# Optimization experiments

Hardware: AMD Instinct MI355X
Metric: run time of the kernel (lower is better)

## Reference

```python
import jax, jax.numpy as jnp
import numpy as np
from itertools import permutations

NODE, BATCH, DIM, STEP = 32, 64, 32, 8
E = NODE * (NODE - 1)          # 992 directed edges (all ordered pairs)
K = 3                          # edge types
MSG_HID = 64; MSG_OUT = 64; N_HID = 64; PRED_LEN = 8


def setup_inputs() -> dict:
    key = jax.random.key(0)
    ks = jax.random.split(key, 12)
    es = jnp.asarray(np.array(list(permutations(range(NODE), 2))).T, dtype=jnp.int32)  # [2, E]
    x = jax.random.normal(ks[0], (BATCH, NODE, DIM, STEP), jnp.float32)
    z = jax.nn.softmax(jax.random.normal(ks[1], (BATCH, E, K), jnp.float32), axis=-1)
    p = lambda k, shape: jax.random.normal(k, shape, jnp.float32) * 0.1
    return dict(
        x=x, z=z, es=es,
        nodes_mask=jnp.zeros((NODE,), jnp.float32),
        edges_mask=jnp.zeros((E,), jnp.float32),
        mask=jnp.zeros((1,), jnp.float32),
        msg_W1=p(ks[2], (K, 2 * DIM, MSG_HID)), msg_b1=jnp.zeros((K, MSG_HID), jnp.float32),
        msg_W2=p(ks[3], (K, MSG_HID, MSG_OUT)), msg_b2=jnp.zeros((K, MSG_OUT), jnp.float32),
        out_W1=p(ks[4], (DIM + MSG_OUT, N_HID)), out_b1=jnp.zeros((N_HID,), jnp.float32),
        out_W2=p(ks[5], (N_HID, N_HID)), out_b2=jnp.zeros((N_HID,), jnp.float32),
        out_W3=p(ks[6], (N_HID, DIM)), out_b3=jnp.zeros((DIM,), jnp.float32),
        ge_Wi=p(ks[7], (3, N_HID, N_HID)), ge_bi=jnp.zeros((3, N_HID), jnp.float32),
        ge_Wh=p(ks[8], (3, N_HID, N_HID)), ge_bh=jnp.zeros((3, N_HID), jnp.float32),
        gn_Wi=p(ks[9], (3, N_HID + DIM, N_HID + DIM)), gn_bi=jnp.zeros((3, N_HID + DIM), jnp.float32),
        gn_Wh=p(ks[10], (3, N_HID + DIM, N_HID + DIM)), gn_bh=jnp.zeros((3, N_HID + DIM), jnp.float32),
    )


def _gru(inp, hid, Wi, bi, Wh, bh):
    # GRUX: state defaults to hidden
    r = jax.nn.sigmoid(inp @ Wi[0] + bi[0] + hid @ Wh[0] + bh[0])
    i = jax.nn.sigmoid(inp @ Wi[1] + bi[1] + hid @ Wh[1] + bh[1])
    n = jnp.tanh(inp @ Wi[2] + bi[2] + r * (hid @ Wh[2] + bh[2]))
    return (1.0 - i) * n + i * hid


def _run(x, z, es, msg_W1, msg_b1, msg_W2, msg_b2,
         out_W1, out_b1, out_W2, out_b2, out_W3, out_b3,
         ge_Wi, ge_bi, ge_Wh, ge_bh, gn_Wi, gn_bi, gn_Wh, gn_bh):
    xp = jnp.transpose(x, (1, 0, 3, 2))   # [node, batch, step, dim]
    zp = jnp.transpose(z, (1, 0, 2))      # [E, batch, K]
    col, row = es[0], es[1]               # 'o2i': col,row = es; aggregate at col
    counts = jnp.clip(jax.ops.segment_sum(jnp.ones((E,), x.dtype), col, num_segments=NODE), 1.0)
    h_node = h_edge = None
    x_m = None
    xs = []
    for t in range(STEP + PRED_LEN):
        x_in = xp[:, :, t, :] if t < STEP else x_m   # [node, batch, dim]
        # edge gather: msg = cat([x[row], x[col]])
        msg = jnp.concatenate([x_in[row], x_in[col]], axis=-1)  # [E, b, 2*dim]
        # per-edge-type 2-layer MLP mixture, weighted by z, normalized by K
        h1 = jax.nn.relu(jnp.einsum('ebi,kih->kebh', msg, msg_W1) + msg_b1[:, None, None, :])
        h2 = jax.nn.relu(jnp.einsum('kebh,kho->kebo', h1, msg_W2) + msg_b2[:, None, None, :])
        msgs = jnp.einsum('kebo,ebk->ebo', h2, zp) / K          # [E, b, msg_out]
        if h_edge is not None:
            msgs = _gru(msgs, h_edge, ge_Wi, ge_bi, ge_Wh, ge_bh)
        # scatter-mean to nodes
        agg = jax.ops.segment_sum(msgs, col, num_segments=NODE) / counts[:, None, None]
        cat = jnp.concatenate([x_in, agg], axis=-1)             # [node, b, dim+msg_out]
        if h_node is not None:
            cat = _gru(cat, h_node, gn_Wi, gn_bi, gn_Wh, gn_bh)
        h = jax.nn.relu(cat @ out_W1 + out_b1)
        h = jax.nn.relu(h @ out_W2 + out_b2)
        delta = h @ out_W3 + out_b3
        x_m = x_in + delta
        h_node, h_edge = cat, msgs
        xs.append(x_m)
    x_hat = jnp.transpose(jnp.stack(xs, axis=2), (1, 0, 3, 2))  # [batch, node, dim, T]
    return x_hat


def reference(x, z, es, nodes_mask, edges_mask, mask,
              msg_W1, msg_b1, msg_W2, msg_b2,
              out_W1, out_b1, out_W2, out_b2, out_W3, out_b3,
              ge_Wi, ge_bi, ge_Wh, ge_bh, gn_Wi, gn_bi, gn_Wh, gn_bh):
    x_hat = _run(x, z, es, msg_W1, msg_b1, msg_W2, msg_b2,
                 out_W1, out_b1, out_W2, out_b2, out_W3, out_b3,
                 ge_Wi, ge_bi, ge_Wh, ge_bh, gn_Wi, gn_bi, gn_Wh, gn_bh)
    return (x_hat[:, :, :, -PRED_LEN:], x_hat, x_hat)
```

## Files before the change

### kernel.cpp

```cpp
#include <hip/hip_runtime.h>
#include <hip/hip_bf16.h>

#define NNODE 32
#define NB    64
#define NDIM  32
#define NSTEP 8
#define NE    992
#define NTT   16

typedef __bf16 bf16;
typedef __attribute__((ext_vector_type(8))) __bf16 bf16x8;
typedef __attribute__((ext_vector_type(4))) __bf16 bf16x4;
typedef __attribute__((ext_vector_type(4))) float  f32x4;

__device__ __forceinline__ f32x4 mfma_bf16(bf16x8 a, bf16x8 b, f32x4 c) {
  return __builtin_amdgcn_mfma_f32_16x16x32_bf16(a, b, c, 0, 0, 0);
}
__device__ __forceinline__ float sigm(float x) { return 1.0f / (1.0f + __expf(-x)); }
__device__ __forceinline__ float tanh_f(float x) {
  x = fminf(fmaxf(x, -15.0f), 15.0f);
  float e = __expf(2.0f * x);
  return (e - 1.0f) / (e + 1.0f);
}

__global__ void prep_weights(
    const float* __restrict__ msgW1, const float* __restrict__ msgW2,
    const float* __restrict__ geWi,  const float* __restrict__ geWh,
    const float* __restrict__ gnWi,  const float* __restrict__ gnWh,
    const float* __restrict__ oW1,   const float* __restrict__ oW2,
    const float* __restrict__ oW3,
    bf16* __restrict__ B1, bf16* __restrict__ B2,
    bf16* __restrict__ GI, bf16* __restrict__ GH,
    bf16* __restrict__ GN,
    bf16* __restrict__ OW1s, bf16* __restrict__ OW2s, bf16* __restrict__ OW3s) {
  int u = blockIdx.x * 256 + threadIdx.x;
  if (u < 12288) {
    int k = u >> 12, i = (u >> 6) & 63, h = u & 63;
// ... 21 lines not shown
    OW1s[((nt * 3 + kf) * 64 + lane) * 8 + j] = (bf16)oW1[v];
  } else if (u < 50176) {
    int v = u - 46080; int i = v >> 6, h = v & 63;
    int kf = i >> 5, quad = (i >> 3) & 3, j = i & 7;
    int nt = h >> 4, lane = quad * 16 + (h & 15);
    OW2s[((nt * 2 + kf) * 64 + lane) * 8 + j] = (bf16)oW2[v];
  } else if (u < 52224) {
    int v = u - 50176; int i = v >> 5, h = v & 31;
    int kf = i >> 5, quad = (i >> 3) & 3, j = i & 7;
    int nt = h >> 4, lane = quad * 16 + (h & 15);
    OW3s[((nt * 2 + kf) * 64 + lane) * 8 + j] = (bf16)oW3[v];
  }
}

__global__ void copy_x(const float* __restrict__ x, float* __restrict__ xf,
                       bf16* __restrict__ xb) {
  int u = blockIdx.x * 256 + threadIdx.x;
  int n = u >> 11, b = (u >> 5) & 63, d = u & 31;
  float v = x[((b * 32 + n) * 32 + d) * 8 + 0];
  xf[u] = v;
  xb[u] = (bf16)v;
}

__global__ __launch_bounds__(512, 4) void edge_step(
    const bf16* __restrict__ xb, const int* __restrict__ es,
    const float* __restrict__ z,
    const bf16* __restrict__ B1, const bf16* __restrict__ B2,
    const float* __restrict__ mb1, const float* __restrict__ mb2,
    const bf16* __restrict__ GI, const bf16* __restrict__ GH,
    const float* __restrict__ gbi, const float* __restrict__ gbh,
    bf16* __restrict__ hed, int t) {
  __shared__ __align__(16) char scrbuf[51200];
  __shared__ float zL[2][64][3];
  __shared__ float biasL[768];
  bf16 (*A)[64][72]   = (bf16(*)[64][72])scrbuf;
  bf16 (*A2)[64][200] = (bf16(*)[64][200])scrbuf;

  int e0 = blockIdx.x * 2, tid = threadIdx.x;
  int c0_ = es[e0],     r0 = es[NE + e0];
  int c1_ = es[e0 + 1], r1 = es[NE + e0 + 1];
  for (int u = tid; u < 768; u += 512)
    biasL[u] = (u < 192) ? mb1[u] : (u < 384) ? mb2[u - 192]
             : (u < 576) ? gbi[u - 384] : gbh[u - 576];
  for (int u = tid; u < 384; u += 512) {
    int pe = u / 192, rem = u % 192, b = rem / 3, k = rem % 3;
    zL[pe][b][k] = z[(b * NE + e0 + pe) * 3 + k];
  }
  for (int u = tid; u < 1024; u += 512) {
    int pe = u >> 9, c = u & 511;
    int b = c >> 3, i8 = c & 7;
    int nrow = pe ? r1 : r0, ncol = pe ? c1_ : c0_;
    const bf16* src = (i8 < 4) ? (xb + nrow * 2048 + b * 32 + i8 * 8)
                               : (xb + ncol * 2048 + b * 32 + (i8 - 4) * 8);
    *(bf16x8*)&A[pe][b][i8 * 8] = *(const bf16x8*)src;
  }
  __syncthreads();
  int wv = tid >> 6, ln = tid & 63, quad = ln >> 4, l16 = ln & 15;
  int rg = wv & 3, cg = wv >> 2;
  int m = rg * 16 + l16;
  bf16x8 af[2][2];
#pragma unroll
  for (int pe = 0; pe < 2; pe++)
#pragma unroll
    for (int kf = 0; kf < 2; kf++)
      af[pe][kf] = *(const bf16x8*)&A[pe][m][kf * 32 + quad * 8];
  __syncthreads();
  f32x4 acc1[2][6];
#pragma unroll
  for (int pe = 0; pe < 2; pe++)
#pragma unroll
    for (int q = 0; q < 6; q++) { f32x4 zz = {0.f,0.f,0.f,0.f}; acc1[pe][q] = zz; }
#pragma unroll
  for (int j = 0; j < 6; j++) {
    int nt = cg * 6 + j;
    bf16x8 w0 = *(const bf16x8*)&B1[(nt * 2 + 0) * 512 + ln * 8];
    bf16x8 w1 = *(const bf16x8*)&B1[(nt * 2 + 1) * 512 + ln * 8];
#pragma unroll
    for (int pe = 0; pe < 2; pe++) {
      acc1[pe][j] = mfma_bf16(af[pe][0], w0, acc1[pe][j]);
      acc1[pe][j] = mfma_bf16(af[pe][1], w1, acc1[pe][j]);
    }
  }
#pragma unroll
  for (int j = 0; j < 6; j++) {
    int nt = cg * 6 + j;
    int n = nt * 16 + l16;
    float bias = biasL[n];
#pragma unroll
    for (int pe = 0; pe < 2; pe++)
#pragma unroll
      for (int r = 0; r < 4; r++) {
        float v = acc1[pe][j][r] + bias;
        A2[pe][rg * 16 + quad * 4 + r][n] = (bf16)(v > 0.f ? v : 0.f);
      }
  }
  __syncthreads();
  f32x4 acc2[2][3][2];
#pragma unroll
  for (int pe = 0; pe < 2; pe++)
#pragma unroll
    for (int kt = 0; kt < 3; kt++)
#pragma unroll
      for (int oi = 0; oi < 2; oi++) { f32x4 zz = {0.f,0.f,0.f,0.f}; acc2[pe][kt][oi] = zz; }
#pragma unroll
  for (int kt = 0; kt < 3; kt++) {
    bf16x8 a2f[2][2];
#pragma unroll
    for (int pe = 0; pe < 2; pe++)
#pragma unroll
      for (int kf = 0; kf < 2; kf++)
        a2f[pe][kf] = *(const bf16x8*)&A2[pe][m][kt * 64 + kf * 32 + quad * 8];
#pragma unroll
    for (int oi = 0; oi < 2; oi++) {
      int ot = cg * 2 + oi;
      bf16x8 w0 = *(const bf16x8*)&B2[kt * 4096 + (ot * 2 + 0) * 512 + ln * 8];
      bf16x8 w1 = *(const bf16x8*)&B2[kt * 4096 + (ot * 2 + 1) * 512 + ln * 8];
#pragma unroll
      for (int pe = 0; pe < 2; pe++) {
        acc2[pe][kt][oi] = mfma_bf16(a2f[pe][0], w0, acc2[pe][kt][oi]);
        acc2[pe][kt][oi] = mfma_bf16(a2f[pe][1], w1, acc2[pe][kt][oi]);
      }
    }
  }
  __syncthreads();
#pragma unroll
  for (int pe = 0; pe < 2; pe++)
#pragma unroll
    for (int r = 0; r < 4; r++) {
      int b = rg * 16 + quad * 4 + r;
      float z0 = zL[pe][b][0], z1 = zL[pe][b][1], z2 = zL[pe][b][2];
#pragma unroll
      for (int oi = 0; oi < 2; oi++) {
        int o = (cg * 2 + oi) * 16 + l16;
        float h0 = acc2[pe][0][oi][r] + biasL[192 + o];       h0 = h0 > 0.f ? h0 : 0.f;
        float h1 = acc2[pe][1][oi][r] + biasL[192 + 64 + o];  h1 = h1 > 0.f ? h1 : 0.f;
        float h2 = acc2[pe][2][oi][r] + biasL[192 + 128 + o]; h2 = h2 > 0.f ? h2 : 0.f;
        A[pe][b][o] = (bf16)((h0 * z0 + h1 * z1 + h2 * z2) * (1.0f / 3.0f));
      }
    }
  if (t > 0) {
    __syncthreads();
    bf16x8 ai[2][2], ah[2][2];
#pragma unroll
    for (int pe = 0; pe < 2; pe++) {
      const bf16* hrow = hed + (e0 + pe) * 4096 + m * 64;
#pragma unroll
      for (int kf = 0; kf < 2; kf++) {
        ai[pe][kf] = *(const bf16x8*)&A[pe][m][kf * 32 + quad * 8];
        ah[pe][kf] = *(const bf16x8*)(hrow + kf * 32 + quad * 8);
      }
    }
#pragma unroll
    for (int oi = 0; oi < 2; oi++) {
      int ot = cg * 2 + oi;
      f32x4 gr[2], gi2[2], gni2[2], gnh2[2];
#pragma unroll
      for (int pe = 0; pe < 2; pe++) {
        f32x4 zz = {0.f,0.f,0.f,0.f};
        gr[pe] = zz; gi2[pe] = zz; gni2[pe] = zz; gnh2[pe] = zz;
      }
#pragma unroll
      for (int g = 0; g < 2; g++) {
        int nt = g * 4 + ot;
        bf16x8 wi0 = *(const bf16x8*)&GI[(nt * 2 + 0) * 512 + ln * 8];
        bf16x8 wi1 = *(const bf16x8*)&GI[(nt * 2 + 1) * 512 + ln * 8];
        bf16x8 wh0 = *(const bf16x8*)&GH[(nt * 2 + 0) * 512 + ln * 8];
        bf16x8 wh1 = *(const bf16x8*)&GH[(nt * 2 + 1) * 512 + ln * 8];
#pragma unroll
        for (int pe = 0; pe < 2; pe++) {
          f32x4 a = g ? gi2[pe] : gr[pe];
          a = mfma_bf16(ai[pe][0], wi0, a);
          a = mfma_bf16(ai[pe][1], wi1, a);
          a = mfma_bf16(ah[pe][0], wh0, a);
          a = mfma_bf16(ah[pe][1], wh1, a);
          if (g) gi2[pe] = a; else gr[pe] = a;
        }
      }
      {
        int nt = 8 + ot;
        bf16x8 wi0 = *(const bf16x8*)&GI[(nt * 2 + 0) * 512 + ln * 8];
        bf16x8 wi1 = *(const bf16x8*)&GI[(nt * 2 + 1) * 512 + ln * 8];
        bf16x8 wh0 = *(const bf16x8*)&GH[(nt * 2 + 0) * 512 + ln * 8];
        bf16x8 wh1 = *(const bf16x8*)&GH[(nt * 2 + 1) * 512 + ln * 8];
#pragma unroll
        for (int pe = 0; pe < 2; pe++) {
          gni2[pe] = mfma_bf16(ai[pe][0], wi0, gni2[pe]);
          gni2[pe] = mfma_bf16(ai[pe][1], wi1, gni2[pe]);
          gnh2[pe] = mfma_bf16(ah[pe][0], wh0, gnh2[pe]);
          gnh2[pe] = mfma_bf16(ah[pe][1], wh1, gnh2[pe]);
        }
      }
#pragma unroll
      for (int pe = 0; pe < 2; pe++)
#pragma unroll
        for (int r = 0; r < 4; r++) {
          int b = rg * 16 + quad * 4 + r;
          int o = ot * 16 + l16;
          float xr = gr[pe][r]   + biasL[384 + o]       + biasL[576 + o];
          float xi = gi2[pe][r]  + biasL[384 + 64 + o]  + biasL[576 + 64 + o];
          float xn = gni2[pe][r] + biasL[384 + 128 + o];
          float hn = gnh2[pe][r] + biasL[576 + 128 + o];
          float rgt = sigm(xr);
          float ig  = sigm(xi);
          float ng  = tanh_f(xn + rgt * hn);
          float hv  = (float)hed[(e0 + pe) * 4096 + b * 64 + o];
          A[pe][b][o] = (bf16)((1.0f - ig) * ng + ig * hv);
        }
    }
  }
  __syncthreads();
  for (int u = tid; u < 1024; u += 512) {
    int pe = u >> 9, c = u & 511;
    int b = c >> 3, j = c & 7;
    *(bf16x8*)(hed + (e0 + pe) * 4096 + b * 64 + j * 8) = *(const bf16x8*)&A[pe][b][j * 8];
  }
}

__global__ __launch_bounds__(256) void node_kernel(
    const float* __restrict__ x, const bf16* __restrict__ hed,
    float* __restrict__ xf, bf16* __restrict__ xb, float* __restrict__ hnode,
    const bf16* __restrict__ GN,
    const float* __restrict__ gnbi, const float* __restrict__ gnbh,
    const bf16* __restrict__ OW1, const float* __restrict__ ob1,
    const bf16* __restrict__ OW2, const float* __restrict__ ob2,
    const bf16* __restrict__ OW3, const float* __restrict__ ob3,
    float* __restrict__ out, int t) {
  __shared__ float aggf[16][64];
  __shared__ float xinf[16][32];
  __shared__ float hvf[16][96];
  __shared__ __align__(16) bf16 c0b[16][112];
  __shared__ __align__(16) bf16 hvb[16][112];
  __shared__ float gsum[2][16][290];
  __shared__ __align__(16) bf16 cnb[16][112];
  __shared__ __align__(16) bf16 s1b[16][112];
  __shared__ __align__(16) bf16 s2b[16][112];
  int nq = blockIdx.x, n = nq >> 2, q = nq & 3;
  int tid = threadIdx.x;
  {
    int r = tid >> 4, o4 = tid & 15;
    const bf16x4* bp = (const bf16x4*)hed + (size_t)n * 31 * 1024 + (q * 16 + r) * 16 + o4;
    float sx = 0.f, sy = 0.f, sz = 0.f, sw = 0.f;
#pragma unroll
    for (int e2 = 0; e2 < 31; e2++) {
      bf16x4 v = bp[e2 * 1024];
      sx += (float)v[0]; sy += (float)v[1]; sz += (float)v[2]; sw += (float)v[3];
    }
    const float inv = 1.0f / 31.0f;
    sx *= inv; sy *= inv; sz *= inv; sw *= inv;
    int o = o4 * 4;
    aggf[r][o] = sx; aggf[r][o + 1] = sy; aggf[r][o + 2] = sz; aggf[r][o + 3] = sw;
    c0b[r][32 + o] = (bf16)sx; c0b[r][33 + o] = (bf16)sy;
    c0b[r][34 + o] = (bf16)sz; c0b[r][35 + o] = (bf16)sw;
  }
  if (tid < 128) {
    int r = tid >> 3, d0 = (tid & 7) * 4;
    int b = q * 16 + r;
#pragma unroll
    for (int k = 0; k < 4; k++) {
      float v = xf[n * 2048 + b * 32 + d0 + k];
      xinf[r][d0 + k] = v;
      c0b[r][d0 + k] = (bf16)v;
    }
  }
  if (t > 0) {
    int r = tid >> 4, cb = (tid & 15) * 6;
    int row = n * 64 + q * 16 + r;
#pragma unroll
    for (int k = 0; k < 6; k++) {
      float v = hnode[row * 96 + cb + k];
      hvf[r][cb + k] = v;
      hvb[r][cb + k] = (bf16)v;
    }
  }
  __syncthreads();
  int wv = tid >> 6, ln = tid & 63, quad = ln >> 4, l16 = ln & 15;
  if (t > 0) {
    int mat = wv >> 1, sel = wv & 1;
    const bf16(*Ab)[112] = mat ? hvb : c0b;
    bf16x8 af[3];
#pragma unroll
    for (int kf = 0; kf < 3; kf++)
      af[kf] = *(const bf16x8*)&Ab[l16][kf * 32 + quad * 8];
    const bf16* W = GN + mat * 27648;
    f32x4 accn[9];
#pragma unroll
    for (int q2 = 0; q2 < 9; q2++) { f32x4 zz = {0.f,0.f,0.f,0.f}; accn[q2] = zz; }
#pragma unroll
    for (int nt2 = 0; nt2 < 9; nt2++) {
      int nt = sel * 9 + nt2;
#pragma unroll
      for (int kf = 0; kf < 3; kf++) {
        bf16x8 bfrag = *(const bf16x8*)&W[((nt * 3 + kf) * 64 + ln) * 8];
        accn[nt2] = mfma_bf16(af[kf], bfrag, accn[nt2]);
      }
    }
#pragma unroll
    for (int nt2 = 0; nt2 < 9; nt2++) {
      int col = (sel * 9 + nt2) * 16 + l16;
#pragma unroll
      for (int rr = 0; rr < 4; rr++)
        gsum[mat][quad * 4 + rr][col] = accn[nt2][rr];
    }
  }
  __syncthreads();
  {
    int r = tid >> 4, cb = (tid & 15) * 6;
    int row = n * 64 + q * 16 + r;
#pragma unroll
    for (int k = 0; k < 6; k++) {
      int c = cb + k;
      float v;
      if (t > 0) {
        float xr = gsum[0][r][c] + gnbi[c] + gsum[1][r][c] + gnbh[c];
        float xi = gsum[0][r][96 + c] + gnbi[96 + c] + gsum[1][r][96 + c] + gnbh[96 + c];
        float xn = gsum[0][r][192 + c] + gnbi[192 + c];
        float hn = gsum[1][r][192 + c] + gnbh[192 + c];
        float rg = sigm(xr);
        float ig = sigm(xi);
        float ng = tanh_f(xn + rg * hn);
        v = (1.0f - ig) * ng + ig * hvf[r][c];
      } else {
        v = (c < 32) ? xinf[r][c] : aggf[r][c - 32];
      }
      cnb[r][c] = (bf16)v;
      hnode[row * 96 + c] = v;
    }
  }
  __syncthreads();
  {
    bf16x8 af[3];
#pragma unroll
    for (int kf = 0; kf < 3; kf++)
      af[kf] = *(const bf16x8*)&cnb[l16][kf * 32 + quad * 8];
    f32x4 accn = {0.f, 0.f, 0.f, 0.f};
#pragma unroll
    for (int kf = 0; kf < 3; kf++) {
      bf16x8 bfrag = *(const bf16x8*)&OW1[((wv * 3 + kf) * 64 + ln) * 8];
      accn = mfma_bf16(af[kf], bfrag, accn);
    }
    int col = wv * 16 + l16;
    float bias = ob1[col];
#pragma unroll
    for (int rr = 0; rr < 4; rr++) {
      float vv = accn[rr] + bias;
      s1b[quad * 4 + rr][col] = (bf16)(vv > 0.f ? vv : 0.f);
    }
  }
  __syncthreads();
  {
    bf16x8 af[2];
#pragma unroll
    for (int kf = 0; kf < 2; kf++)
      af[kf] = *(const bf16x8*)&s1b[l16][kf * 32 + quad * 8];
    f32x4 accn = {0.f, 0.f, 0.f, 0.f};
#pragma unroll
    for (int kf = 0; kf < 2; kf++) {
      bf16x8 bfrag = *(const bf16x8*)&OW2[((wv * 2 + kf) * 64 + ln) * 8];
      accn = mfma_bf16(af[kf], bfrag, accn);
    }
    int col = wv * 16 + l16;
    float bias = ob2[col];
#pragma unroll
    for (int rr = 0; rr < 4; rr++) {
      float vv = accn[rr] + bias;
      s2b[quad * 4 + rr][col] = (bf16)(vv > 0.f ? vv : 0.f);
    }
  }
  __syncthreads();
  if (wv < 2) {
    bf16x8 af[2];
#pragma unroll
    for (int kf = 0; kf < 2; kf++)
      af[kf] = *(const bf16x8*)&s2b[l16][kf * 32 + quad * 8];
    f32x4 accn = {0.f, 0.f, 0.f, 0.f};
#pragma unroll
    for (int kf = 0; kf < 2; kf++) {
      bf16x8 bfrag = *(const bf16x8*)&OW3[((wv * 2 + kf) * 64 + ln) * 8];
      accn = mfma_bf16(af[kf], bfrag, accn);
    }
    int d = wv * 16 + l16;
    float bias = ob3[d];
#pragma unroll
    for (int rr = 0; rr < 4; rr++) {
      int r = quad * 4 + rr;
      int b = q * 16 + r;
      float xm = xinf[r][d] + accn[rr] + bias;
      int base = (b * 32 + n) * 32 + d;
      out[524288 + base * 16 + t] = xm;
      out[1572864 + base * 16 + t] = xm;
      if (t >= NSTEP) out[base * 8 + (t - NSTEP)] = xm;
      float vnext = (t + 1 < NSTEP) ? x[base * 8 + (t + 1)] : xm;
      xf[n * 2048 + b * 32 + d] = vnext;
      xb[n * 2048 + b * 32 + d] = (bf16)vnext;
    }
  }
}

extern "C" void kernel_launch(void* const* d_in, const int* in_sizes, int n_in,
                              void* d_out, int out_size, void* d_ws, size_t ws_size,
                              hipStream_t stream) {
  const float* x     = (const float*)d_in[0];
  const float* z     = (const float*)d_in[1];
  const int*   es    = (const int*)d_in[2];
  const float* msgW1 = (const float*)d_in[6];
  const float* msgb1 = (const float*)d_in[7];
  const float* msgW2 = (const float*)d_in[8];
  const float* msgb2 = (const float*)d_in[9];
  const float* oW1   = (const float*)d_in[10];
  const float* ob1   = (const float*)d_in[11];
// ... 12 lines not shown
  float* out = (float*)d_out;

  char* p = (char*)d_ws;
  bf16*  hed   = (bf16*)p;   p += (size_t)NE * 4096 * 2;
  float* xf    = (float*)p;  p += 65536 * 4;
  bf16*  xb    = (bf16*)p;   p += 65536 * 2;
  float* hnode = (float*)p;  p += 196608 * 4;
  bf16*  B1sw  = (bf16*)p;   p += 12288 * 2;
  bf16*  B2sw  = (bf16*)p;   p += 12288 * 2;
  bf16*  GIsw  = (bf16*)p;   p += 12288 * 2;
  bf16*  GHsw  = (bf16*)p;   p += 12288 * 2;
  bf16*  GNsw  = (bf16*)p;   p += 55296 * 2;
  bf16*  OW1s  = (bf16*)p;   p += 6144 * 2;
  bf16*  OW2s  = (bf16*)p;   p += 4096 * 2;
  bf16*  OW3s  = (bf16*)p;   p += 2048 * 2;

  prep_weights<<<204, 256, 0, stream>>>(msgW1, msgW2, geWi, geWh, gnWi, gnWh,
                                        oW1, oW2, oW3,
                                        B1sw, B2sw, GIsw, GHsw, GNsw,
                                        OW1s, OW2s, OW3s);
  copy_x<<<256, 256, 0, stream>>>(x, xf, xb);

  for (int t = 0; t < NTT; t++) {
    edge_step<<<NE / 2, 512, 0, stream>>>(xb, es, z, B1sw, B2sw, msgb1, msgb2,
                                          GIsw, GHsw, gebi, gebh, hed, t);
    node_kernel<<<128, 256, 0, stream>>>(x, hed, xf, xb, hnode, GNsw, gnbi, gnbh,
                                         OW1s, ob1, OW2s, ob2, OW3s, ob3,
                                         out, t);
  }
}
```

Measured before the change: 614.2 us.

## Fuse per-step edge and node kernels into one persistent kernel with grid barrier

Replaces the 32 alternating edge_step/node_kernel launches with a single persistent kernel of 496 blocks that loops over all 16 timesteps and synchronises through a hierarchical atomic grid barrier. Node work is folded into the same blocks, and biases plus the z values are loaded into shared memory once for the whole loop. This removes per-launch overhead and inter-kernel gaps. The cost is that all blocks must be co-resident, which risks deadlock if occupancy is insufficient, and every block pays for barrier spin-waiting.

```diff
diff --git a/kernel.cpp b/kernel.cpp
--- a/kernel.cpp
+++ b/kernel.cpp
@@ -7,6 +7,7 @@
 #define NSTEP 8
 #define NE    992
 #define NTT   16
+#define NBLK  496
 
 typedef __bf16 bf16;
 typedef __attribute__((ext_vector_type(8))) __bf16 bf16x8;
@@ -21,6 +22,26 @@
   x = fminf(fmaxf(x, -15.0f), 15.0f);
   float e = __expf(2.0f * x);
   return (e - 1.0f) / (e + 1.0f);
+}
+
+__device__ __forceinline__ void grid_barrier(unsigned* bar, unsigned phase) {
+  __syncthreads();
+  if (threadIdx.x == 0) {
+    __threadfence();
+    unsigned* leafc = bar + (blockIdx.x & 15) * 32;
+    unsigned* rootc = bar + 512;
+    unsigned* gen   = bar + 544;
+    unsigned a = __hip_atomic_fetch_add(leafc, 1u, __ATOMIC_ACQ_REL, __HIP_MEMORY_SCOPE_AGENT);
+    if (a + 1 == phase * 31u) {
+      unsigned rb = __hip_atomic_fetch_add(rootc, 1u, __ATOMIC_ACQ_REL, __HIP_MEMORY_SCOPE_AGENT);
+      if (rb + 1 == phase * 16u)
+        __hip_atomic_store(gen, phase, __ATOMIC_RELEASE, __HIP_MEMORY_SCOPE_AGENT);
+    }
+    while (__hip_atomic_load(gen, __ATOMIC_RELAXED, __HIP_MEMORY_SCOPE_AGENT) < phase)
+      __builtin_amdgcn_s_sleep(2);
+    __threadfence();
+  }
+  __syncthreads();
 }
 
 __global__ void prep_weights(
@@ -72,385 +93,421 @@
 }
 
 __global__ void copy_x(const float* __restrict__ x, float* __restrict__ xf,
-                       bf16* __restrict__ xb) {
+                       bf16* __restrict__ xb, unsigned* __restrict__ bar) {
   int u = blockIdx.x * 256 + threadIdx.x;
+  if (u < 576) bar[u] = 0u;
   int n = u >> 11, b = (u >> 5) & 63, d = u & 31;
   float v = x[((b * 32 + n) * 32 + d) * 8 + 0];
   xf[u] = v;
   xb[u] = (bf16)v;
 }
 
-__global__ __launch_bounds__(512, 4) void edge_step(
-    const bf16* __restrict__ xb, const int* __restrict__ es,
+__global__ __launch_bounds__(512, 4) void fused_rnn(
+    const float* __restrict__ x, const int* __restrict__ es,
     const float* __restrict__ z,
     const bf16* __restrict__ B1, const bf16* __restrict__ B2,
     const float* __restrict__ mb1, const float* __restrict__ mb2,
     const bf16* __restrict__ GI, const bf16* __restrict__ GH,
     const float* __restrict__ gbi, const float* __restrict__ gbh,
-    bf16* __restrict__ hed, int t) {
-  __shared__ __align__(16) char scrbuf[51200];
-  __shared__ float zL[2][64][3];
-  __shared__ float biasL[768];
-  bf16 (*A)[64][72]   = (bf16(*)[64][72])scrbuf;
-  bf16 (*A2)[64][200] = (bf16(*)[64][200])scrbuf;
-
-  int e0 = blockIdx.x * 2, tid = threadIdx.x;
-  int c0_ = es[e0],     r0 = es[NE + e0];
-  int c1_ = es[e0 + 1], r1 = es[NE + e0 + 1];
-  for (int u = tid; u < 768; u += 512)
-    biasL[u] = (u < 192) ? mb1[u] : (u < 384) ? mb2[u - 192]
-             : (u < 576) ? gbi[u - 384] : gbh[u - 576];
-  for (int u = tid; u < 384; u += 512) {
-    int pe = u / 192, rem = u % 192, b = rem / 3, k = rem % 3;
-    zL[pe][b][k] = z[(b * NE + e0 + pe) * 3 + k];
-  }
-  for (int u = tid; u < 1024; u += 512) {
-    int pe = u >> 9, c = u & 511;
-    int b = c >> 3, i8 = c & 7;
-    int nrow = pe ? r1 : r0, ncol = pe ? c1_ : c0_;
-    const bf16* src = (i8 < 4) ? (xb + nrow * 2048 + b * 32 + i8 * 8)
-                               : (xb + ncol * 2048 + b * 32 + (i8 - 4) * 8);
-    *(bf16x8*)&A[pe][b][i8 * 8] = *(const bf16x8*)src;
-  }
-  __syncthreads();
-  int wv = tid >> 6, ln = tid & 63, quad = ln >> 4, l16 = ln & 15;
-  int rg = wv & 3, cg = wv >> 2;
-  int m = rg * 16 + l16;
-  bf16x8 af[2][2];
-#pragma unroll
-  for (int pe = 0; pe < 2; pe++)
-#pragma unroll
-    for (int kf = 0; kf < 2; kf++)
-      af[pe][kf] = *(const bf16x8*)&A[pe][m][kf * 32 + quad * 8];
-  __syncthreads();
-  f32x4 acc1[2][6];
-#pragma unroll
-  for (int pe = 0; pe < 2; pe++)
-#pragma unroll
-    for (int q = 0; q < 6; q++) { f32x4 zz = {0.f,0.f,0.f,0.f}; acc1[pe][q] = zz; }
-#pragma unroll
-  for (int j = 0; j < 6; j++) {
-    int nt = cg * 6 + j;
-    bf16x8 w0 = *(const bf16x8*)&B1[(nt * 2 + 0) * 512 + ln * 8];
-    bf16x8 w1 = *(const bf16x8*)&B1[(nt * 2 + 1) * 512 + ln * 8];
-#pragma unroll
-    for (int pe = 0; pe < 2; pe++) {
-      acc1[pe][j] = mfma_bf16(af[pe][0], w0, acc1[pe][j]);
-      acc1[pe][j] = mfma_bf16(af[pe][1], w1, acc1[pe][j]);
-    }
-  }
-#pragma unroll
-  for (int j = 0; j < 6; j++) {
-    int nt = cg * 6 + j;
-    int n = nt * 16 + l16;
-    float bias = biasL[n];
-#pragma unroll
-    for (int pe = 0; pe < 2; pe++)
-#pragma unroll
-      for (int r = 0; r < 4; r++) {
-        float v = acc1[pe][j][r] + bias;
-        A2[pe][rg * 16 + quad * 4 + r][n] = (bf16)(v > 0.f ? v : 0.f);
-      }
-  }
-  __syncthreads();
-  f32x4 acc2[2][3][2];
-#pragma unroll
-  for (int pe = 0; pe < 2; pe++)
-#pragma unroll
-    for (int kt = 0; kt < 3; kt++)
-#pragma unroll
-      for (int oi = 0; oi < 2; oi++) { f32x4 zz = {0.f,0.f,0.f,0.f}; acc2[pe][kt][oi] = zz; }
-#pragma unroll
-  for (int kt = 0; kt < 3; kt++) {
-    bf16x8 a2f[2][2];
-#pragma unroll
-    for (int pe = 0; pe < 2; pe++)
-#pragma unroll
-      for (int kf = 0; kf < 2; kf++)
-        a2f[pe][kf] = *(const bf16x8*)&A2[pe][m][kt * 64 + kf * 32 + quad * 8];
-#pragma unroll
-    for (int oi = 0; oi < 2; oi++) {
-      int ot = cg * 2 + oi;
-      bf16x8 w0 = *(const bf16x8*)&B2[kt * 4096 + (ot * 2 + 0) * 512 + ln * 8];
-      bf16x8 w1 = *(const bf16x8*)&B2[kt * 4096 + (ot * 2 + 1) * 512 + ln * 8];
-#pragma unroll
-      for (int pe = 0; pe < 2; pe++) {
-        acc2[pe][kt][oi] = mfma_bf16(a2f[pe][0], w0, acc2[pe][kt][oi]);
-        acc2[pe][kt][oi] = mfma_bf16(a2f[pe][1], w1, acc2[pe][kt][oi]);
-      }
-    }
-  }
-  __syncthreads();
-#pragma unroll
-  for (int pe = 0; pe < 2; pe++)
-#pragma unroll
-    for (int r = 0; r < 4; r++) {
-      int b = rg * 16 + quad * 4 + r;
-      float z0 = zL[pe][b][0], z1 = zL[pe][b][1], z2 = zL[pe][b][2];
-#pragma unroll
-      for (int oi = 0; oi < 2; oi++) {
-        int o = (cg * 2 + oi) * 16 + l16;
-        float h0 = acc2[pe][0][oi][r] + biasL[192 + o];       h0 = h0 > 0.f ? h0 : 0.f;
-        float h1 = acc2[pe][1][oi][r] + biasL[192 + 64 + o];  h1 = h1 > 0.f ? h1 : 0.f;
-        float h2 = acc2[pe][2][oi][r] + biasL[192 + 128 + o]; h2 = h2 > 0.f ? h2 : 0.f;
-        A[pe][b][o] = (bf16)((h0 * z0 + h1 * z1 + h2 * z2) * (1.0f / 3.0f));
-      }
-    }
-  if (t > 0) {
-    __syncthreads();
-    bf16x8 ai[2][2], ah[2][2];
-#pragma unroll
-    for (int pe = 0; pe < 2; pe++) {
-      const bf16* hrow = hed + (e0 + pe) * 4096 + m * 64;
-#pragma unroll
-      for (int kf = 0; kf < 2; kf++) {
-        ai[pe][kf] = *(const bf16x8*)&A[pe][m][kf * 32 + quad * 8];
-        ah[pe][kf] = *(const bf16x8*)(hrow + kf * 32 + quad * 8);
-      }
-    }
-#pragma unroll
-    for (int oi = 0; oi < 2; oi++) {
-      int ot = cg * 2 + oi;
-      f32x4 gr[2], gi2[2], gni2[2], gnh2[2];
-#pragma unroll
-      for (int pe = 0; pe < 2; pe++) {
-        f32x4 zz = {0.f,0.f,0.f,0.f};
-        gr[pe] = zz; gi2[pe] = zz; gni2[pe] = zz; gnh2[pe] = zz;
-      }
-#pragma unroll
-      for (int g = 0; g < 2; g++) {
-        int nt = g * 4 + ot;
-        bf16x8 wi0 = *(const bf16x8*)&GI[(nt * 2 + 0) * 512 + ln * 8];
-        bf16x8 wi1 = *(const bf16x8*)&GI[(nt * 2 + 1) * 512 + ln * 8];
-        bf16x8 wh0 = *(const bf16x8*)&GH[(nt * 2 + 0) * 512 + ln * 8];
-        bf16x8 wh1 = *(const bf16x8*)&GH[(nt * 2 + 1) * 512 + ln * 8];
-#pragma unroll
-        for (int pe = 0; pe < 2; pe++) {
-          f32x4 a = g ? gi2[pe] : gr[pe];
-          a = mfma_bf16(ai[pe][0], wi0, a);
-          a = mfma_bf16(ai[pe][1], wi1, a);
-          a = mfma_bf16(ah[pe][0], wh0, a);
-          a = mfma_bf16(ah[pe][1], wh1, a);
-          if (g) gi2[pe] = a; else gr[pe] = a;
-        }
-      }
-      {
-        int nt = 8 + ot;
-        bf16x8 wi0 = *(const bf16x8*)&GI[(nt * 2 + 0) * 512 + ln * 8];
-        bf16x8 wi1 = *(const bf16x8*)&GI[(nt * 2 + 1) * 512 + ln * 8];
-        bf16x8 wh0 = *(const bf16x8*)&GH[(nt * 2 + 0) * 512 + ln * 8];
-        bf16x8 wh1 = *(const bf16x8*)&GH[(nt * 2 + 1) * 512 + ln * 8];
-#pragma unroll
-        for (int pe = 0; pe < 2; pe++) {
-          gni2[pe] = mfma_bf16(ai[pe][0], wi0, gni2[pe]);
-          gni2[pe] = mfma_bf16(ai[pe][1], wi1, gni2[pe]);
-          gnh2[pe] = mfma_bf16(ah[pe][0], wh0, gnh2[pe]);
-          gnh2[pe] = mfma_bf16(ah[pe][1], wh1, gnh2[pe]);
-        }
-      }
-#pragma unroll
-      for (int pe = 0; pe < 2; pe++)
-#pragma unroll
-        for (int r = 0; r < 4; r++) {
-          int b = rg * 16 + quad * 4 + r;
-          int o = ot * 16 + l16;
-          float xr = gr[pe][r]   + biasL[384 + o]       + biasL[576 + o];
-          float xi = gi2[pe][r]  + biasL[384 + 64 + o]  + biasL[576 + 64 + o];
-          float xn = gni2[pe][r] + biasL[384 + 128 + o];
-          float hn = gnh2[pe][r] + biasL[576 + 128 + o];
-          float rgt = sigm(xr);
-          float ig  = sigm(xi);
-          float ng  = tanh_f(xn + rgt * hn);
-          float hv  = (float)hed[(e0 + pe) * 4096 + b * 64 + o];
-          A[pe][b][o] = (bf16)((1.0f - ig) * ng + ig * hv);
-        }
-    }
-  }
-  __syncthreads();
-  for (int u = tid; u < 1024; u += 512) {
-    int pe = u >> 9, c = u & 511;
-    int b = c >> 3, j = c & 7;
-    *(bf16x8*)(hed + (e0 + pe) * 4096 + b * 64 + j * 8) = *(const bf16x8*)&A[pe][b][j * 8];
-  }
-}
-
-__global__ __launch_bounds__(256) void node_kernel(
-    const float* __restrict__ x, const bf16* __restrict__ hed,
-    float* __restrict__ xf, bf16* __restrict__ xb, float* __restrict__ hnode,
     const bf16* __restrict__ GN,
     const float* __restrict__ gnbi, const float* __restrict__ gnbh,
     const bf16* __restrict__ OW1, const float* __restrict__ ob1,
     const bf16* __restrict__ OW2, const float* __restrict__ ob2,
     const bf16* __restrict__ OW3, const float* __restrict__ ob3,
-    float* __restrict__ out, int t) {
-  __shared__ float aggf[16][64];
-  __shared__ float xinf[16][32];
-  __shared__ float hvf[16][96];
-  __shared__ __align__(16) bf16 c0b[16][112];
-  __shared__ __align__(16) bf16 hvb[16][112];
-  __shared__ float gsum[2][16][290];
-  __shared__ __align__(16) bf16 cnb[16][112];
-  __shared__ __align__(16) bf16 s1b[16][112];
-  __shared__ __align__(16) bf16 s2b[16][112];
-  int nq = blockIdx.x, n = nq >> 2, q = nq & 3;
-  int tid = threadIdx.x;
-  {
-    int r = tid >> 4, o4 = tid & 15;
-    const bf16x4* bp = (const bf16x4*)hed + (size_t)n * 31 * 1024 + (q * 16 + r) * 16 + o4;
-    float sx = 0.f, sy = 0.f, sz = 0.f, sw = 0.f;
-#pragma unroll
-    for (int e2 = 0; e2 < 31; e2++) {
-      bf16x4 v = bp[e2 * 1024];
-      sx += (float)v[0]; sy += (float)v[1]; sz += (float)v[2]; sw += (float)v[3];
-    }
-    const float inv = 1.0f / 31.0f;
-    sx *= inv; sy *= inv; sz *= inv; sw *= inv;
-    int o = o4 * 4;
-    aggf[r][o] = sx; aggf[r][o + 1] = sy; aggf[r][o + 2] = sz; aggf[r][o + 3] = sw;
-    c0b[r][32 + o] = (bf16)sx; c0b[r][33 + o] = (bf16)sy;
-    c0b[r][34 + o] = (bf16)sz; c0b[r][35 + o] = (bf16)sw;
+    bf16* __restrict__ hed, float* __restrict__ xf, bf16* __restrict__ xb,
+    float* __restrict__ hnode, float* __restrict__ out,
+    unsigned* __restrict__ bar) {
+  __shared__ __align__(16) char scrbuf[51200];
+  __shared__ float zL[2][64][3];
+  __shared__ float biasL[1504];
+  __shared__ __align__(16) bf16 hedL[2][64][72];
+
+  bf16 (*A)[64][72]   = (bf16(*)[64][72])scrbuf;
+  bf16 (*A2)[64][200] = (bf16(*)[64][200])scrbuf;
+  float (*xinf)[32]  = (float(*)[32])(scrbuf + 0);
+  float (*hvf)[96]   = (float(*)[96])(scrbuf + 2048);
+  bf16  (*c0b)[112]  = (bf16(*)[112])(scrbuf + 8192);
+  bf16  (*hvb)[112]  = (bf16(*)[112])(scrbuf + 11776);
+  float (*gri)[194]  = (float(*)[194])(scrbuf + 15360);
+  float (*gni)[98]   = (float(*)[98])(scrbuf + 27776);
+  float (*gnh)[98]   = (float(*)[98])(scrbuf + 34048);
+  bf16  (*cnb)[112]  = (bf16(*)[112])(scrbuf + 40320);
+  bf16  (*s1b)[112]  = (bf16(*)[112])(scrbuf + 43904);
+  bf16  (*s2b)[112]  = (bf16(*)[112])(scrbuf + 47488);
+  float (*aggPB)[64] = (float(*)[64])(scrbuf + 15360);
+
+  int bid = blockIdx.x, tid = threadIdx.x;
+  int e0 = bid * 2;
+  int c0_ = es[e0],     r0 = es[NE + e0];
+  int c1_ = es[e0 + 1], r1 = es[NE + e0 + 1];
+  int wv = tid >> 6, ln = tid & 63, quad = ln >> 4, l16 = ln & 15;
+  int rg = wv & 3, cg = wv >> 2;
+  int m = rg * 16 + l16;
+
+  for (int u = tid; u < 1504; u += 512) {
+    float v;
+    if      (u < 192)  v = mb1[u];
+    else if (u < 384)  v = mb2[u - 192];
+    else if (u < 576)  v = gbi[u - 384];
+    else if (u < 768)  v = gbh[u - 576];
+    else if (u < 1056) v = gnbi[u - 768];
+    else if (u < 1344) v = gnbh[u - 1056];
+    else if (u < 1408) v = ob1[u - 1344];
+    else if (u < 1472) v = ob2[u - 1408];
+    else               v = ob3[u - 1472];
+    biasL[u] = v;
   }
-  if (tid < 128) {
-    int r = tid >> 3, d0 = (tid & 7) * 4;
-    int b = q * 16 + r;
-#pragma unroll
-    for (int k = 0; k < 4; k++) {
-      float v = xf[n * 2048 + b * 32 + d0 + k];
-      xinf[r][d0 + k] = v;
-      c0b[r][d0 + k] = (bf16)v;
-    }
+  for (int u = tid; u < 384; u += 512) {
+    int pe = u / 192, rem = u % 192, b = rem / 3, k = rem % 3;
+    zL[pe][b][k] = z[(b * NE + e0 + pe) * 3 + k];
   }
-  if (t > 0) {
-    int r = tid >> 4, cb = (tid & 15) * 6;
-    int row = n * 64 + q * 16 + r;
-#pragma unroll
-    for (int k = 0; k < 6; k++) {
-      float v = hnode[row * 96 + cb + k];
-      hvf[r][cb + k] = v;
-      hvb[r][cb + k] = (bf16)v;
-    }
-  }
-  __syncthreads();
-  int wv = tid >> 6, ln = tid & 63, quad = ln >> 4, l16 = ln & 15;
-  if (t > 0) {
-    int mat = wv >> 1, sel = wv & 1;
-    const bf16(*Ab)[112] = mat ? hvb : c0b;
-    bf16x8 af[3];
-#pragma unroll
-    for (int kf = 0; kf < 3; kf++)
-      af[kf] = *(const bf16x8*)&Ab[l16][kf * 32 + quad * 8];
-    const bf16* W = GN + mat * 27648;
-    f32x4 accn[9];
-#pragma unroll
-    for (int q2 = 0; q2 < 9; q2++) { f32x4 zz = {0.f,0.f,0.f,0.f}; accn[q2] = zz; }
-#pragma unroll
-    for (int nt2 = 0; nt2 < 9; nt2++) {
-      int nt = sel * 9 + nt2;
-#pragma unroll
-      for (int kf = 0; kf < 3; kf++) {
-        bf16x8 bfrag = *(const bf16x8*)&W[((nt * 3 + kf) * 64 + ln) * 8];
-        accn[nt2] = mfma_bf16(af[kf], bfrag, accn[nt2]);
-      }
-    }
-#pragma unroll
-    for (int nt2 = 0; nt2 < 9; nt2++) {
-      int col = (sel * 9 + nt2) * 16 + l16;
-#pragma unroll
-      for (int rr = 0; rr < 4; rr++)
-        gsum[mat][quad * 4 + rr][col] = accn[nt2][rr];
-    }
-  }
-  __syncthreads();
-  {
-    int r = tid >> 4, cb = (tid & 15) * 6;
-    int row = n * 64 + q * 16 + r;
-#pragma unroll
-    for (int k = 0; k < 6; k++) {
-      int c = cb + k;
-      float v;
+
+  unsigned phase = 0;
+  for (int t = 0; t < NTT; t++) {
+    for (int u = tid; u < 1024; u += 512) {
+      int pe = u >> 9, c = u & 511;
+      int b = c >> 3, i8 = c & 7;
+      int nrow = pe ? r1 : r0, ncol = pe ? c1_ : c0_;
+      const bf16* src = (i8 < 4) ? (xb + nrow * 2048 + b * 32 + i8 * 8)
+                                 : (xb + ncol * 2048 + b * 32 + (i8 - 4) * 8);
+      *(bf16x8*)&A[pe][b][i8 * 8] = *(const bf16x8*)src;
+    }
+    __syncthreads();
+    bf16x8 af[2][2];
+#pragma unroll
+    for (int pe = 0; pe < 2; pe++)
+#pragma unroll
+      for (int kf = 0; kf < 2; kf++)
+        af[pe][kf] = *(const bf16x8*)&A[pe][m][kf * 32 + quad * 8];
+    __syncthreads();
+    f32x4 acc1[2][6];
+#pragma unroll
+    for (int pe = 0; pe < 2; pe++)
+#pragma unroll
+      for (int q2 = 0; q2 < 6; q2++) { f32x4 zz = {0.f,0.f,0.f,0.f}; acc1[pe][q2] = zz; }
+#pragma unroll
+    for (int j = 0; j < 6; j++) {
+      int nt = cg * 6 + j;
+      bf16x8 w0 = *(const bf16x8*)&B1[(nt * 2 + 0) * 512 + ln * 8];
+      bf16x8 w1 = *(const bf16x8*)&B1[(nt * 2 + 1) * 512 + ln * 8];
+#pragma unroll
+      for (int pe = 0; pe < 2; pe++) {
+        acc1[pe][j] = mfma_bf16(af[pe][0], w0, acc1[pe][j]);
+        acc1[pe][j] = mfma_bf16(af[pe][1], w1, acc1[pe][j]);
+      }
+    }
+#pragma unroll
+    for (int j = 0; j < 6; j++) {
+      int nt = cg * 6 + j;
+      int n2 = nt * 16 + l16;
+      float bias = biasL[n2];
+#pragma unroll
+      for (int pe = 0; pe < 2; pe++)
+#pragma unroll
+        for (int r = 0; r < 4; r++) {
+          float v = acc1[pe][j][r] + bias;
+          A2[pe][rg * 16 + quad * 4 + r][n2] = (bf16)(v > 0.f ? v : 0.f);
+        }
+    }
+    __syncthreads();
+    f32x4 acc2[2][3][2];
+#pragma unroll
+    for (int pe = 0; pe < 2; pe++)
+#pragma unroll
+      for (int kt = 0; kt < 3; kt++)
+#pragma unroll
+        for (int oi = 0; oi < 2; oi++) { f32x4 zz = {0.f,0.f,0.f,0.f}; acc2[pe][kt][oi] = zz; }
+#pragma unroll
+    for (int kt = 0; kt < 3; kt++) {
+      bf16x8 a2f[2][2];
+#pragma unroll
+      for (int pe = 0; pe < 2; pe++)
+#pragma unroll
+        for (int kf = 0; kf < 2; kf++)
+          a2f[pe][kf] = *(const bf16x8*)&A2[pe][m][kt * 64 + kf * 32 + quad * 8];
+#pragma unroll
+      for (int oi = 0; oi < 2; oi++) {
+        int ot = cg * 2 + oi;
+        bf16x8 w0 = *(const bf16x8*)&B2[kt * 4096 + (ot * 2 + 0) * 512 + ln * 8];
+        bf16x8 w1 = *(const bf16x8*)&B2[kt * 4096 + (ot * 2 + 1) * 512 + ln * 8];
+#pragma unroll
+        for (int pe = 0; pe < 2; pe++) {
+          acc2[pe][kt][oi] = mfma_bf16(a2f[pe][0], w0, acc2[pe][kt][oi]);
+          acc2[pe][kt][oi] = mfma_bf16(a2f[pe][1], w1, acc2[pe][kt][oi]);
+        }
+      }
+    }
+    __syncthreads();
+#pragma unroll
+    for (int pe = 0; pe < 2; pe++)
+#pragma unroll
+      for (int r = 0; r < 4; r++) {
+        int b = rg * 16 + quad * 4 + r;
+        float z0 = zL[pe][b][0], z1 = zL[pe][b][1], z2 = zL[pe][b][2];
+#pragma unroll
+        for (int oi = 0; oi < 2; oi++) {
+          int o = (cg * 2 + oi) * 16 + l16;
+          float h0 = acc2[pe][0][oi][r] + biasL[192 + o];       h0 = h0 > 0.f ? h0 : 0.f;
+          float h1 = acc2[pe][1][oi][r] + biasL[192 + 64 + o];  h1 = h1 > 0.f ? h1 : 0.f;
+          float h2 = acc2[pe][2][oi][r] + biasL[192 + 128 + o]; h2 = h2 > 0.f ? h2 : 0.f;
+          A[pe][b][o] = (bf16)((h0 * z0 + h1 * z1 + h2 * z2) * (1.0f / 3.0f));
+        }
+      }
+    if (t > 0) {
+      __syncthreads();
+      bf16x8 ai[2][2], ah[2][2];
+#pragma unroll
+      for (int pe = 0; pe < 2; pe++)
+#pragma unroll
+        for (int kf = 0; kf < 2; kf++) {
+          ai[pe][kf] = *(const bf16x8*)&A[pe][m][kf * 32 + quad * 8];
+          ah[pe][kf] = *(const bf16x8*)&hedL[pe][m][kf * 32 + quad * 8];
+        }
+#pragma unroll
+      for (int oi = 0; oi < 2; oi++) {
+        int ot = cg * 2 + oi;
+        f32x4 gr[2], gi2[2], gni2[2], gnh2[2];
+#pragma unroll
+        for (int pe = 0; pe < 2; pe++) {
+          f32x4 zz = {0.f,0.f,0.f,0.f};
+          gr[pe] = zz; gi2[pe] = zz; gni2[pe] = zz; gnh2[pe] = zz;
+        }
+#pragma unroll
+        for (int g = 0; g < 2; g++) {
+          int nt = g * 4 + ot;
+          bf16x8 wi0 = *(const bf16x8*)&GI[(nt * 2 + 0) * 512 + ln * 8];
+          bf16x8 wi1 = *(const bf16x8*)&GI[(nt * 2 + 1) * 512 + ln * 8];
+          bf16x8 wh0 = *(const bf16x8*)&GH[(nt * 2 + 0) * 512 + ln * 8];
+          bf16x8 wh1 = *(const bf16x8*)&GH[(nt * 2 + 1) * 512 + ln * 8];
+#pragma unroll
+          for (int pe = 0; pe < 2; pe++) {
+            f32x4 a = g ? gi2[pe] : gr[pe];
+            a = mfma_bf16(ai[pe][0], wi0, a);
+            a = mfma_bf16(ai[pe][1], wi1, a);
+            a = mfma_bf16(ah[pe][0], wh0, a);
+            a = mfma_bf16(ah[pe][1], wh1, a);
+            if (g) gi2[pe] = a; else gr[pe] = a;
+          }
+        }
+        {
+          int nt = 8 + ot;
+          bf16x8 wi0 = *(const bf16x8*)&GI[(nt * 2 + 0) * 512 + ln * 8];
+          bf16x8 wi1 = *(const bf16x8*)&GI[(nt * 2 + 1) * 512 + ln * 8];
+          bf16x8 wh0 = *(const bf16x8*)&GH[(nt * 2 + 0) * 512 + ln * 8];
+          bf16x8 wh1 = *(const bf16x8*)&GH[(nt * 2 + 1) * 512 + ln * 8];
+#pragma unroll
+          for (int pe = 0; pe < 2; pe++) {
+            gni2[pe] = mfma_bf16(ai[pe][0], wi0, gni2[pe]);
+            gni2[pe] = mfma_bf16(ai[pe][1], wi1, gni2[pe]);
+            gnh2[pe] = mfma_bf16(ah[pe][0], wh0, gnh2[pe]);
+            gnh2[pe] = mfma_bf16(ah[pe][1], wh1, gnh2[pe]);
+          }
+        }
+#pragma unroll
+        for (int pe = 0; pe < 2; pe++)
+#pragma unroll
+          for (int r = 0; r < 4; r++) {
+            int b = rg * 16 + quad * 4 + r;
+            int o = ot * 16 + l16;
+            float xr = gr[pe][r]   + biasL[384 + o]       + biasL[576 + o];
+            float xi = gi2[pe][r]  + biasL[384 + 64 + o]  + biasL[576 + 64 + o];
+            float xn = gni2[pe][r] + biasL[384 + 128 + o];
+            float hn = gnh2[pe][r] + biasL[576 + 128 + o];
+            float rgt = sigm(xr);
+            float ig  = sigm(xi);
+            float ng  = tanh_f(xn + rgt * hn);
+            float hv  = (float)hedL[pe][b][o];
+            A[pe][b][o] = (bf16)((1.0f - ig) * ng + ig * hv);
+          }
+      }
+    }
+    __syncthreads();
+    for (int u = tid; u < 1024; u += 512) {
+      int pe = u >> 9, c = u & 511;
+      int b = c >> 3, j = c & 7;
+      bf16x8 v = *(const bf16x8*)&A[pe][b][j * 8];
+      *(bf16x8*)(hed + (e0 + pe) * 4096 + b * 64 + j * 8) = v;
+      *(bf16x8*)&hedL[pe][b][j * 8] = v;
+    }
+
+    phase++; grid_barrier(bar, phase);
+
+    if (bid < 128) {
+      int n = bid >> 2, q = bid & 3;
+      int half = tid >> 8;
+      int r4 = (tid >> 4) & 15, o4 = tid & 15;
+      float sx = 0.f, sy = 0.f, sz2 = 0.f, sw = 0.f;
+      {
+        const bf16x4* bp = (const bf16x4*)hed + (size_t)n * 31 * 1024 +
+                           (q * 16 + r4) * 16 + o4 + (half ? (size_t)16384 : 0);
+        int ecnt = half ? 15 : 16;
+        for (int e2 = 0; e2 < ecnt; e2++) {
+          bf16x4 v = bp[(size_t)e2 * 1024];
+          sx += (float)v[0]; sy += (float)v[1]; sz2 += (float)v[2]; sw += (float)v[3];
+        }
+        if (half) {
+          f32x4 pv = {sx, sy, sz2, sw};
+          *(f32x4*)&aggPB[r4][o4 * 4] = pv;
+        }
+      }
+      if (tid < 128) {
+        int r = tid >> 3, d0 = (tid & 7) * 4;
+        int b = q * 16 + r;
+#pragma unroll
+        for (int k = 0; k < 4; k++) {
+          float v = xf[n * 2048 + b * 32 + d0 + k];
+          xinf[r][d0 + k] = v;
+          c0b[r][d0 + k] = (bf16)v;
+          if (t == 0) hnode[(n * 64 + b) * 96 + d0 + k] = v;
+        }
+      }
+      if (t > 0 && tid < 256) {
+        int r = tid >> 4, cb = (tid & 15) * 6;
+        int row = n * 64 + q * 16 + r;
+#pragma unroll
+        for (int k = 0; k < 6; k++) {
+          float v = hnode[row * 96 + cb + k];
+          hvf[r][cb + k] = v;
+          hvb[r][cb + k] = (bf16)v;
+        }
+      }
+      __syncthreads();
+      if (tid < 256) {
+        f32x4 pv = *(const f32x4*)&aggPB[r4][o4 * 4];
+        const float inv = 1.0f / 31.0f;
+        sx = (sx + pv[0]) * inv; sy = (sy + pv[1]) * inv;
+        sz2 = (sz2 + pv[2]) * inv; sw = (sw + pv[3]) * inv;
+        int o = o4 * 4;
+        c0b[r4][32 + o] = (bf16)sx; c0b[r4][33 + o] = (bf16)sy;
+        c0b[r4][34 + o] = (bf16)sz2; c0b[r4][35 + o] = (bf16)sw;
+        if (t == 0) {
+          int row = n * 64 + q * 16 + r4;
+          hnode[row * 96 + 32 + o] = sx;  hnode[row * 96 + 33 + o] = sy;
+          hnode[row * 96 + 34 + o] = sz2; hnode[row * 96 + 35 + o] = sw;
+        }
+      }
+      __syncthreads();
       if (t > 0) {
-        float xr = gsum[0][r][c] + gnbi[c] + gsum[1][r][c] + gnbh[c];
-        float xi = gsum[0][r][96 + c] + gnbi[96 + c] + gsum[1][r][96 + c] + gnbh[96 + c];
-        float xn = gsum[0][r][192 + c] + gnbi[192 + c];
-        float hn = gsum[1][r][192 + c] + gnbh[192 + c];
-        float rg = sigm(xr);
-        float ig = sigm(xi);
-        float ng = tanh_f(xn + rg * hn);
-        v = (1.0f - ig) * ng + ig * hvf[r][c];
-      } else {
-        v = (c < 32) ? xinf[r][c] : aggf[r][c - 32];
-      }
-      cnb[r][c] = (bf16)v;
-      hnode[row * 96 + c] = v;
-    }
-  }
-  __syncthreads();
-  {
-    bf16x8 af[3];
-#pragma unroll
-    for (int kf = 0; kf < 3; kf++)
-      af[kf] = *(const bf16x8*)&cnb[l16][kf * 32 + quad * 8];
-    f32x4 accn = {0.f, 0.f, 0.f, 0.f};
-#pragma unroll
-    for (int kf = 0; kf < 3; kf++) {
-      bf16x8 bfrag = *(const bf16x8*)&OW1[((wv * 3 + kf) * 64 + ln) * 8];
-      accn = mfma_bf16(af[kf], bfrag, accn);
-    }
-    int col = wv * 16 + l16;
-    float bias = ob1[col];
-#pragma unroll
-    for (int rr = 0; rr < 4; rr++) {
-      float vv = accn[rr] + bias;
-      s1b[quad * 4 + rr][col] = (bf16)(vv > 0.f ? vv : 0.f);
-    }
-  }
-  __syncthreads();
-  {
-    bf16x8 af[2];
-#pragma unroll
-    for (int kf = 0; kf < 2; kf++)
-      af[kf] = *(const bf16x8*)&s1b[l16][kf * 32 + quad * 8];
-    f32x4 accn = {0.f, 0.f, 0.f, 0.f};
-#pragma unroll
-    for (int kf = 0; kf < 2; kf++) {
-      bf16x8 bfrag = *(const bf16x8*)&OW2[((wv * 2 + kf) * 64 + ln) * 8];
-      accn = mfma_bf16(af[kf], bfrag, accn);
-    }
-    int col = wv * 16 + l16;
-    float bias = ob2[col];
-#pragma unroll
-    for (int rr = 0; rr < 4; rr++) {
-      float vv = accn[rr] + bias;
-      s2b[quad * 4 + rr][col] = (bf16)(vv > 0.f ? vv : 0.f);
-    }
-  }
-  __syncthreads();
-  if (wv < 2) {
-    bf16x8 af[2];
-#pragma unroll
-    for (int kf = 0; kf < 2; kf++)
-      af[kf] = *(const bf16x8*)&s2b[l16][kf * 32 + quad * 8];
-    f32x4 accn = {0.f, 0.f, 0.f, 0.f};
-#pragma unroll
-    for (int kf = 0; kf < 2; kf++) {
-      bf16x8 bfrag = *(const bf16x8*)&OW3[((wv * 2 + kf) * 64 + ln) * 8];
-      accn = mfma_bf16(af[kf], bfrag, accn);
-    }
-    int d = wv * 16 + l16;
-    float bias = ob3[d];
-#pragma unroll
-    for (int rr = 0; rr < 4; rr++) {
-      int r = quad * 4 + rr;
-      int b = q * 16 + r;
-      float xm = xinf[r][d] + accn[rr] + bias;
-      int base = (b * 32 + n) * 32 + d;
-      out[524288 + base * 16 + t] = xm;
-      out[1572864 + base * 16 + t] = xm;
-      if (t >= NSTEP) out[base * 8 + (t - NSTEP)] = xm;
-      float vnext = (t + 1 < NSTEP) ? x[base * 8 + (t + 1)] : xm;
-      xf[n * 2048 + b * 32 + d] = vnext;
-      xb[n * 2048 + b * 32 + d] = (bf16)vnext;
-    }
+        bf16x8 a0[3], a1[3];
+#pragma unroll
+        for (int kf = 0; kf < 3; kf++) {
+          a0[kf] = *(const bf16x8*)&c0b[l16][kf * 32 + quad * 8];
+          a1[kf] = *(const bf16x8*)&hvb[l16][kf * 32 + quad * 8];
+        }
+        for (int nt = wv; nt < 18; nt += 8) {
+          f32x4 acc0 = {0.f,0.f,0.f,0.f}, accB = {0.f,0.f,0.f,0.f};
+#pragma unroll
+          for (int kf = 0; kf < 3; kf++) {
+            bf16x8 w0 = *(const bf16x8*)&GN[((nt * 3 + kf) * 64 + ln) * 8];
+            bf16x8 w1 = *(const bf16x8*)&GN[27648 + ((nt * 3 + kf) * 64 + ln) * 8];
+            acc0 = mfma_bf16(a0[kf], w0, acc0);
+            accB = mfma_bf16(a1[kf], w1, accB);
+          }
+          int colb = nt * 16 + l16;
+          if (nt < 12) {
+#pragma unroll
+            for (int rr = 0; rr < 4; rr++)
+              gri[quad * 4 + rr][colb] = acc0[rr] + accB[rr];
+          } else {
+#pragma unroll
+            for (int rr = 0; rr < 4; rr++) {
+              gni[quad * 4 + rr][colb - 192] = acc0[rr];
+              gnh[quad * 4 + rr][colb - 192] = accB[rr];
+            }
+          }
+        }
+      }
+      __syncthreads();
+      if (t > 0 && tid < 256) {
+        int r = tid >> 4, cb = (tid & 15) * 6;
+        int row = n * 64 + q * 16 + r;
+#pragma unroll
+        for (int k = 0; k < 6; k++) {
+          int c = cb + k;
+          float xr = gri[r][c]      + biasL[768 + c]      + biasL[1056 + c];
+          float xi = gri[r][96 + c] + biasL[864 + c]      + biasL[1152 + c];
+          float xn = gni[r][c] + biasL[960 + c];
+          float hn = gnh[r][c] + biasL[1248 + c];
+          float rg2 = sigm(xr);
+          float ig = sigm(xi);
+          float ng = tanh_f(xn + rg2 * hn);
+          float v = (1.0f - ig) * ng + ig * hvf[r][c];
+          cnb[r][c] = (bf16)v;
+          hnode[row * 96 + c] = v;
+        }
+      }
+      __syncthreads();
+      const bf16 (*CN)[112] = (t > 0) ? (const bf16(*)[112])cnb : (const bf16(*)[112])c0b;
+      if (wv < 4) {
+        bf16x8 af3[3];
+#pragma unroll
+        for (int kf = 0; kf < 3; kf++)
+          af3[kf] = *(const bf16x8*)&CN[l16][kf * 32 + quad * 8];
+        f32x4 accn = {0.f,0.f,0.f,0.f};
+#pragma unroll
+        for (int kf = 0; kf < 3; kf++) {
+          bf16x8 bfrag = *(const bf16x8*)&OW1[((wv * 3 + kf) * 64 + ln) * 8];
+          accn = mfma_bf16(af3[kf], bfrag, accn);
+        }
+        int col = wv * 16 + l16;
+        float bias = biasL[1344 + col];
+#pragma unroll
+        for (int rr = 0; rr < 4; rr++) {
+          float vv = accn[rr] + bias;
+          s1b[quad * 4 + rr][col] = (bf16)(vv > 0.f ? vv : 0.f);
+        }
+      }
+      __syncthreads();
+      if (wv < 4) {
+        bf16x8 af2[2];
+#pragma unroll
+        for (int kf = 0; kf < 2; kf++)
+          af2[kf] = *(const bf16x8*)&s1b[l16][kf * 32 + quad * 8];
+        f32x4 accn = {0.f,0.f,0.f,0.f};
+#pragma unroll
+        for (int kf = 0; kf < 2; kf++) {
+          bf16x8 bfrag = *(const bf16x8*)&OW2[((wv * 2 + kf) * 64 + ln) * 8];
+          accn = mfma_bf16(af2[kf], bfrag, accn);
+        }
+        int col = wv * 16 + l16;
+        float bias = biasL[1408 + col];
+#pragma unroll
+        for (int rr = 0; rr < 4; rr++) {
+          float vv = accn[rr] + bias;
+          s2b[quad * 4 + rr][col] = (bf16)(vv > 0.f ? vv : 0.f);
+        }
+      }
+      __syncthreads();
+      if (wv < 2) {
+        bf16x8 af2[2];
+#pragma unroll
+        for (int kf = 0; kf < 2; kf++)
+          af2[kf] = *(const bf16x8*)&s2b[l16][kf * 32 + quad * 8];
+        f32x4 accn = {0.f,0.f,0.f,0.f};
+#pragma unroll
+        for (int kf = 0; kf < 2; kf++) {
+          bf16x8 bfrag = *(const bf16x8*)&OW3[((wv * 2 + kf) * 64 + ln) * 8];
+          accn = mfma_bf16(af2[kf], bfrag, accn);
+        }
+        int d = wv * 16 + l16;
+        float bias = biasL[1472 + d];
+#pragma unroll
+        for (int rr = 0; rr < 4; rr++) {
+          int r = quad * 4 + rr;
+          int b = q * 16 + r;
+          float xm = xinf[r][d] + accn[rr] + bias;
+          int base = (b * 32 + n) * 32 + d;
+          out[524288 + base * 16 + t] = xm;
+          out[1572864 + base * 16 + t] = xm;
+          if (t >= NSTEP) out[base * 8 + (t - NSTEP)] = xm;
+          float vnext = (t + 1 < NSTEP) ? x[base * 8 + (t + 1)] : xm;
+          xf[n * 2048 + b * 32 + d] = vnext;
+          xb[n * 2048 + b * 32 + d] = (bf16)vnext;
+        }
+      }
+    }
+
+    if (t < NTT - 1) { phase++; grid_barrier(bar, phase); }
   }
 }
 
@@ -493,18 +550,17 @@
   bf16*  OW1s  = (bf16*)p;   p += 6144 * 2;
   bf16*  OW2s  = (bf16*)p;   p += 4096 * 2;
   bf16*  OW3s  = (bf16*)p;   p += 2048 * 2;
+  unsigned* bar = (unsigned*)p; p += 576 * 4;
 
   prep_weights<<<204, 256, 0, stream>>>(msgW1, msgW2, geWi, geWh, gnWi, gnWh,
                                         oW1, oW2, oW3,
                                         B1sw, B2sw, GIsw, GHsw, GNsw,
                                         OW1s, OW2s, OW3s);
-  copy_x<<<256, 256, 0, stream>>>(x, xf, xb);
-
-  for (int t = 0; t < NTT; t++) {
-    edge_step<<<NE / 2, 512, 0, stream>>>(xb, es, z, B1sw, B2sw, msgb1, msgb2,
-                                          GIsw, GHsw, gebi, gebh, hed, t);
-    node_kernel<<<128, 256, 0, stream>>>(x, hed, xf, xb, hnode, GNsw, gnbi, gnbh,
-                                         OW1s, ob1, OW2s, ob2, OW3s, ob3,
-                                         out, t);
-  }
-}
+  copy_x<<<256, 256, 0, stream>>>(x, xf, xb, bar);
+
+  fused_rnn<<<NBLK, 512, 0, stream>>>(x, es, z, B1sw, B2sw, msgb1, msgb2,
+                                      GIsw, GHsw, gebi, gebh,
+                                      GNsw, gnbi, gnbh,
+                                      OW1s, ob1, OW2s, ob2, OW3s, ob3,
+                                      hed, xf, xb, hnode, out, bar);
+}
```

New measurement: 2.107 ms. 243% more time.
